# Optimization experiments

Hardware: AMD Instinct MI355X
Metric: run time of the kernel (lower is better)

The kernel has to match this reference:

```python
import jax, jax.numpy as jnp
import numpy as np

H_DIM = 1024


def setup_inputs() -> dict:
    key = jax.random.key(0)
    k1, k2, k3, k4 = jax.random.split(key, 4)
    B, S, H = 8, 2048, H_DIM
    scale = 1.0 / np.sqrt(H)
    x = jax.random.normal(k1, (B, S, H), dtype=jnp.float32)
    attention_mask = jnp.ones((B, S), dtype=jnp.int32)
    wq = jax.random.normal(k2, (H, H), dtype=jnp.float32) * scale
    wk = jax.random.normal(k3, (H, H), dtype=jnp.float32) * scale
    wv = jax.random.normal(k4, (H, H), dtype=jnp.float32) * scale
    return {"x": x, "attention_mask": attention_mask, "wq": wq, "wk": wk, "wv": wv}


def reference(x, attention_mask, wq, wk, wv):
    # x: [B,S,H]; torch Linear(no bias): y = x @ W.T
    B, S, H = x.shape
    q = jnp.einsum('bsh,oh->bso', x, wq)
    k = jnp.einsum('bsh,oh->bso', x, wk)
    v = jnp.einsum('bsh,oh->bso', x, wv)
    qk = jnp.einsum('bqh,bkh->bqk', q, k) / jnp.sqrt(jnp.asarray(H, jnp.float32))
    # causal: mask positions where key index > query index (strict upper triangle)
    causal = jnp.triu(jnp.ones((S, S), dtype=bool), k=1)  # [S,S]
    m = attention_mask.astype(bool)                        # [B,S]
    allowed = m[:, None, :] & m[:, :, None]                # d & e: key-valid AND query-valid
    condition = causal[None, :, :] | jnp.logical_not(allowed)
    qk = jnp.where(condition, -jnp.inf, qk)
    att = jax.nn.softmax(qk, axis=-1)
    att = jnp.where(jnp.isnan(att), 0.0, att)  # fully-masked rows -> 0
    return jnp.einsum('bqk,bkh->bqh', att, v)
```

## Files before the change

### kernel.cpp

```cpp
#include <hip/hip_runtime.h>
#include <stdint.h>

typedef unsigned short u16;
typedef __bf16 bf16x8 __attribute__((ext_vector_type(8)));
typedef float f32x4 __attribute__((ext_vector_type(4)));
typedef u16 ushort8 __attribute__((ext_vector_type(8)));

#define SB 8
#define SS 2048
#define SH 1024
#define MTOT (SB*SS)
#define LOG2E 1.44269504088896f
#define SEXP (1.44269504088896f/32.f)
#define NEG_INF (-__builtin_inff())

typedef __attribute__((address_space(3))) void lds_void;
typedef __attribute__((address_space(1))) const void gbl_void;

__device__ __forceinline__ float bf2f(u16 v) {
    union { unsigned int u; float f; } x; x.u = ((unsigned int)v) << 16; return x.f;
}
__device__ __forceinline__ u16 f2bf(float f) {
    unsigned int u = __builtin_bit_cast(unsigned int, f);
    u += 0x7fffu + ((u >> 16) & 1u);
    return (u16)(u >> 16);
}

__global__ void cvt_f32_bf16(const float* __restrict__ in, u16* __restrict__ out, int n8) {
    int i = blockIdx.x * 256 + threadIdx.x;
    if (i >= n8) return;
    const float4* p = (const float4*)(in + (size_t)i * 8);
    float4 a = p[0], b = p[1];
    ushort8 r;
    r[0] = f2bf(a.x); r[1] = f2bf(a.y); r[2] = f2bf(a.z); r[3] = f2bf(a.w);
    r[4] = f2bf(b.x); r[5] = f2bf(b.y); r[6] = f2bf(b.z); r[7] = f2bf(b.w);
    *(ushort8*)(out + (size_t)i * 8) = r;
}

__device__ __forceinline__ void stage_tile(const u16* __restrict__ g, int ld,
                                           u16* lds, int w, int l) {
#pragma unroll
    for (int i = 0; i < 4; i++) {
        int chunk = i * 4 + w;
        int r = chunk * 8 + (l >> 3);
        int c = (l & 7) * 8;
        __builtin_amdgcn_global_load_lds(
            (gbl_void*)(g + (size_t)r * ld + c),
            (lds_void*)(lds + chunk * 512), 16, 0, 0);
    }
}

__device__ __forceinline__ void mfma_tile(const u16* As, const u16* Bs,
                                          f32x4 acc[4][4], int w, int l) {
    int wr = (w >> 1) * 64, wc = (w & 1) * 64;
    int lr = l & 15, lk = (l >> 4) * 8;
#pragma unroll
    for (int kk = 0; kk < 2; kk++) {
        bf16x8 af[4], bb[4];
#pragma unroll
        for (int m = 0; m < 4; m++)
            af[m] = *(const bf16x8*)(const void*)(As + (wr + m * 16 + lr) * 64 + kk * 32 + lk);
#pragma unroll
        for (int n = 0; n < 4; n++)
            bb[n] = *(const bf16x8*)(const void*)(Bs + (wc + n * 16 + lr) * 64 + kk * 32 + lk);
#pragma unroll
        for (int m = 0; m < 4; m++)
#pragma unroll
            for (int n = 0; n < 4; n++)
                acc[m][n] = __builtin_amdgcn_mfma_f32_16x16x32_bf16(af[m], bb[n], acc[m][n], 0, 0, 0);
    }
}

#define QNT 16

#define STAGE8(gbase, ld, bufidx, h, t) do {                                          \
    const u16* _g = (gbase) + ((size_t)((h)*128 + srow)) * (ld) + (size_t)(t)*64 + scol; \
    u16* _d = &lds4[bufidx][((h)*128 + (w << 3)) * 64];                               \
    __builtin_amdgcn_global_load_lds((gbl_void*)_g, (lds_void*)_d, 16, 0, 0);         \
    __builtin_amdgcn_global_load_lds((gbl_void*)(_g + (size_t)64*(ld)),               \
                                     (lds_void*)(_d + 64*64), 16, 0, 0);              \
} while (0)

#define LDA8(mf, kkv) (*(const bf16x8*)(const void*)(Ab + (wr + (mf)*16 + rrow)*64 + rk##kkv))
#define LDB8(nf, kkv) (*(const bf16x8*)(const void*)(Bb + (wc + (nf)*16 + rrow)*64 + rk##kkv))

#define MFMA_PAIR(mf, A0, A1)                                                          \
    acc[mf][0] = __builtin_amdgcn_mfma_f32_16x16x32_bf16(A0, b00, acc[mf][0], 0,0,0);  \
    acc[mf][0] = __builtin_amdgcn_mfma_f32_16x16x32_bf16(A1, b01, acc[mf][0], 0,0,0);  \
    acc[mf][1] = __builtin_amdgcn_mfma_f32_16x16x32_bf16(A0, b10, acc[mf][1], 0,0,0);  \
    acc[mf][1] = __builtin_amdgcn_mfma_f32_16x16x32_bf16(A1, b11, acc[mf][1], 0,0,0);  \
    acc[mf][2] = __builtin_amdgcn_mfma_f32_16x16x32_bf16(A0, b20, acc[mf][2], 0,0,0);  \
    acc[mf][2] = __builtin_amdgcn_mfma_f32_16x16x32_bf16(A1, b21, acc[mf][2], 0,0,0);  \
    acc[mf][3] = __builtin_amdgcn_mfma_f32_16x16x32_bf16(A0, b30, acc[mf][3], 0,0,0);  \
    acc[mf][3] = __builtin_amdgcn_mfma_f32_16x16x32_bf16(A1, b31, acc[mf][3], 0,0,0);

#define PH_BAR_MID()                       \
    __builtin_amdgcn_sched_barrier(0);     \
    __builtin_amdgcn_s_barrier();          \
    __builtin_amdgcn_sched_barrier(0);

#define PH_BAR_END()                       \
    __builtin_amdgcn_sched_barrier(0);     \
    __builtin_amdgcn_s_barrier();          \
    __builtin_amdgcn_sched_barrier(0);

__global__ __launch_bounds__(512, 2) void gemm_qkv8(
    const u16* __restrict__ X, const u16* __restrict__ W,
    u16* __restrict__ Q, u16* __restrict__ Kd, u16* __restrict__ Vd) {
    __shared__ u16 lds4[4][256 * 64];

    int tid = threadIdx.x, w = tid >> 6, l = tid & 63;
    int bid = blockIdx.x;
    int wg = (bid & 7) * 96 + (bid >> 3);
    int mt = wg / 12, nb = wg % 12;

    const u16* gA = X + (size_t)mt * 256 * SH;
    const u16* gB = W + (size_t)nb * 256 * SH;

    int srow = (w << 3) + (l >> 3);
    int scol = (((l & 7) ^ ((l >> 3) & 7)) << 3);
    int wr = (w >> 2) * 128, wc = (w & 3) * 64;
    int rrow = l & 15;
    int rk0 = (((l >> 4) ^ (l & 7)) << 3);
    int rk1 = (((4 + (l >> 4)) ^ (l & 7)) << 3);

    f32x4 acc[8][4];
#pragma unroll
    for (int m = 0; m < 8; m++)
#pragma unroll
        for (int n = 0; n < 4; n++) acc[m][n] = (f32x4){0.f, 0.f, 0.f, 0.f};

    STAGE8(gA, SH, 0, 0, 0); STAGE8(gA, SH, 0, 1, 0);
    STAGE8(gB, SH, 2, 0, 0); STAGE8(gB, SH, 2, 1, 0);
    STAGE8(gB, SH, 3, 0, 1); STAGE8(gB, SH, 3, 1, 1);
    asm volatile("s_waitcnt vmcnt(4)" ::: "memory");
    __builtin_amdgcn_s_barrier();
    __builtin_amdgcn_sched_barrier(0);

    for (int t = 0; t < QNT; ++t) {
        const int p = t & 1;
        const u16* Ab = &lds4[p][0];
        const u16* Bb = &lds4[2 + p][0];

        bf16x8 b00 = LDB8(0, 0), b01 = LDB8(0, 1), b10 = LDB8(1, 0), b11 = LDB8(1, 1);
        bf16x8 b20 = LDB8(2, 0), b21 = LDB8(2, 1), b30 = LDB8(3, 0), b31 = LDB8(3, 1);
        {
            bf16x8 a00 = LDA8(0, 0), a01 = LDA8(0, 1), a10 = LDA8(1, 0), a11 = LDA8(1, 1);
            if (t + 1 < QNT) STAGE8(gA, SH, (t + 1) & 1, 0, t + 1);
            PH_BAR_MID();
            __builtin_amdgcn_s_setprio(1);
            MFMA_PAIR(0, a00, a01);
            MFMA_PAIR(1, a10, a11);
            __builtin_amdgcn_s_setprio(0);
            PH_BAR_END();
        }
        {
            bf16x8 a00 = LDA8(2, 0), a01 = LDA8(2, 1), a10 = LDA8(3, 0), a11 = LDA8(3, 1);
            if (t + 1 < QNT) STAGE8(gA, SH, (t + 1) & 1, 1, t + 1);
            PH_BAR_MID();
            __builtin_amdgcn_s_setprio(1);
            MFMA_PAIR(2, a00, a01);
            MFMA_PAIR(3, a10, a11);
            __builtin_amdgcn_s_setprio(0);
            PH_BAR_END();
        }
        {
            bf16x8 a00 = LDA8(4, 0), a01 = LDA8(4, 1), a10 = LDA8(5, 0), a11 = LDA8(5, 1);
            if (t + 2 < QNT) STAGE8(gB, SH, 2 + (t & 1), 0, t + 2);
            PH_BAR_MID();
            __builtin_amdgcn_s_setprio(1);
            MFMA_PAIR(4, a00, a01);
            MFMA_PAIR(5, a10, a11);
            __builtin_amdgcn_s_setprio(0);
            PH_BAR_END();
        }
        {
            bf16x8 a00 = LDA8(6, 0), a01 = LDA8(6, 1), a10 = LDA8(7, 0), a11 = LDA8(7, 1);
            if (t + 2 < QNT) STAGE8(gB, SH, 2 + (t & 1), 1, t + 2);
            if (t + 2 < QNT)      asm volatile("s_waitcnt vmcnt(4)" ::: "memory");
            else if (t + 1 < QNT) asm volatile("s_waitcnt vmcnt(0)" ::: "memory");
            PH_BAR_MID();
            __builtin_amdgcn_s_setprio(1);
            MFMA_PAIR(6, a00, a01);
            MFMA_PAIR(7, a10, a11);
            __builtin_amdgcn_s_setprio(0);
            PH_BAR_END();
        }
    }

    u16* outp = (nb < 4 ? Q : (nb < 8 ? Kd : Vd));
    int colbase = (nb & 3) * 256 + wc;
    size_t rowbase = (size_t)mt * 256 + wr;
    int g = l >> 4, c = l & 15;
#pragma unroll
    for (int mf = 0; mf < 8; mf++)
#pragma unroll
        for (int j = 0; j < 4; j++) {
            size_t ro = (rowbase + mf * 16 + g * 4 + j) * SH;
#pragma unroll
            for (int nf = 0; nf < 4; nf++)
                outp[ro + colbase + nf * 16 + c] = f2bf(acc[mf][nf][j]);
        }
}

__global__ void transpose_v(const u16* __restrict__ V, u16* __restrict__ Vt) {
    __shared__ u16 t[64][80];
    int s0 = blockIdx.x * 64, o0 = blockIdx.y * 64, b = blockIdx.z;
    const u16* src = V + (size_t)b * SS * SH;
    u16* dst = Vt + (size_t)b * SH * SS;
    int tid = threadIdx.x;
#pragma unroll
    for (int it = 0; it < 2; it++) {
        int idx = it * 256 + tid;
        int r = idx >> 3, gq = idx & 7;
        *(ushort8*)&t[r][gq * 8] = *(const ushort8*)&src[(size_t)(s0 + r) * SH + o0 + gq * 8];
    }
    __syncthreads();
#pragma unroll
    for (int it = 0; it < 2; it++) {
        int idx = it * 256 + tid;
        int rr = idx >> 3, cc = idx & 7;
        ushort8 v;
#pragma unroll
        for (int e = 0; e < 8; e++) v[e] = t[cc * 8 + e][rr];
        *(ushort8*)&dst[(size_t)(o0 + rr) * SS + s0 + cc * 8] = v;
    }
}

__global__ __launch_bounds__(256, 2) void gemm_scores(
    const u16* __restrict__ Q, const u16* __restrict__ K,
    u16* __restrict__ P, float* __restrict__ lb,
    const int* __restrict__ amask) {
    __shared__ u16 As[128 * 64];
    __shared__ u16 Bs[128 * 64];
    int tid = threadIdx.x, w = tid >> 6, l = tid & 63;
    int b = blockIdx.y, t = blockIdx.x;
    int qt = (int)((sqrtf(8.f * (float)t + 1.f) - 1.f) * 0.5f);
    while ((qt + 1) * (qt + 2) / 2 <= t) qt++;
    while (qt * (qt + 1) / 2 > t) qt--;
    int kt = t - qt * (qt + 1) / 2;
    const u16* A = Q + ((size_t)b * SS + (size_t)qt * 128) * SH;
    const u16* Bt = K + ((size_t)b * SS + (size_t)kt * 128) * SH;
    f32x4 acc[4][4];
#pragma unroll
    for (int m = 0; m < 4; m++)
#pragma unroll
        for (int n = 0; n < 4; n++) acc[m][n] = (f32x4){0.f, 0.f, 0.f, 0.f};
    for (int k0 = 0; k0 < SH; k0 += 64) {
        stage_tile(A + k0, SH, As, w, l);
        stage_tile(Bt + k0, SH, Bs, w, l);
        __syncthreads();
        mfma_tile(As, Bs, acc, w, l);
        __syncthreads();
    }
    int wr = (w >> 1) * 64, wc = (w & 1) * 64, g = l >> 4, c = l & 15;
    int q0 = qt * 128 + wr;
    int k0w = kt * 128 + wc;
    int cglob = kt * 2 + (w & 1);
    u16* Pb = P + (size_t)b * SS * SS;
    float* lbb = lb + (size_t)b * SS * 32;
    int kg[4], kv[4];
#pragma unroll
    for (int n = 0; n < 4; n++) { kg[n] = k0w + n * 16 + c; kv[n] = amask[b * SS + kg[n]]; }
#pragma unroll
    for (int m = 0; m < 4; m++) {
#pragma unroll
        for (int j = 0; j < 4; j++) {
            int qg = q0 + m * 16 + g * 4 + j;
            float sv[4]; float ls = 0.f;
#pragma unroll
            for (int n = 0; n < 4; n++) {
                bool ok = (kg[n] <= qg) && (kv[n] != 0);
                float p = ok ? exp2f(acc[m][n][j] * SEXP) : 0.f;
                sv[n] = p; ls += p;
            }
#pragma unroll
            for (int d = 1; d < 16; d <<= 1) ls += __shfl_xor(ls, d, 64);
            size_t prow = (size_t)qg * SS;
#pragma unroll
            for (int n = 0; n < 4; n++) Pb[prow + kg[n]] = f2bf(sv[n]);
            if (c == 0) lbb[(size_t)qg * 32 + cglob] = ls;
        }
    }
}

__global__ void combine_inv(const float* __restrict__ lb,
                            float* __restrict__ sb, const int* __restrict__ amask) {
    int row = blockIdx.x * 4 + (threadIdx.x >> 6);
    int l = threadIdx.x & 63;
    int b = row >> 11, q = row & 2047;
    int cmax = q >> 6;
    float L = (l < 32 && l <= cmax) ? lb[(size_t)row * 32 + l] : 0.f;
#pragma unroll
    for (int d = 1; d < 64; d <<= 1) L += __shfl_xor(L, d, 64);
    if (l == 0) {
        int qv = amask[b * SS + q];
        sb[row] = (qv != 0 && L > 0.f) ? 1.0f / L : 0.f;
    }
}

__global__ __launch_bounds__(256, 2) void gemm_pv(
    const u16* __restrict__ P, const u16* __restrict__ Vt,
    const float* __restrict__ sb, float* __restrict__ Out) {
    __shared__ u16 As[128 * 64];
    __shared__ u16 Bs[128 * 64];
    int tid = threadIdx.x, w = tid >> 6, l = tid & 63;
    int b = blockIdx.y;
    int qt = blockIdx.x >> 3, nt = blockIdx.x & 7;
    const u16* Ab = P + (size_t)b * SS * SS + (size_t)qt * 128 * SS;
    const u16* Bt = Vt + (size_t)b * SH * SS + (size_t)nt * 128 * SS;
    int ksize = (qt + 1) * 128;
    f32x4 acc[4][4];
#pragma unroll
    for (int m = 0; m < 4; m++)
#pragma unroll
        for (int n = 0; n < 4; n++) acc[m][n] = (f32x4){0.f, 0.f, 0.f, 0.f};
    for (int k0 = 0; k0 < ksize; k0 += 64) {
        stage_tile(Ab + k0, SS, As, w, l);
        stage_tile(Bt + k0, SS, Bs, w, l);
        __syncthreads();
        mfma_tile(As, Bs, acc, w, l);
        __syncthreads();
    }
    const float* sbq = sb + (size_t)b * SS + (size_t)qt * 128;
    float* out = Out + ((size_t)b * SS + (size_t)qt * 128) * SH + nt * 128;
    int wr = (w >> 1) * 64, wc = (w & 1) * 64, g = l >> 4, c = l & 15;
#pragma unroll
    for (int m = 0; m < 4; m++)
#pragma unroll
        for (int j = 0; j < 4; j++) {
            int row = wr + m * 16 + g * 4 + j;
            float scl = sbq[row];
            size_t ro = (size_t)row * SH;
#pragma unroll
            for (int n = 0; n < 4; n++)
                out[ro + wc + n * 16 + c] = acc[m][n][j] * scl;
        }
}

extern "C" void kernel_launch(void* const* d_in, const int* in_sizes, int n_in,
                              void* d_out, int out_size, void* d_ws, size_t ws_size,
                              hipStream_t stream) {
    const float* x = (const float*)d_in[0];
    const int* amask = (const int*)d_in[1];
    const float* wq = (const float*)d_in[2];
    const float* wk = (const float*)d_in[3];
    const float* wv = (const float*)d_in[4];
    float* out = (float*)d_out;

    const size_t SZQ = (size_t)MTOT * SH * 2;
    const size_t SZSTAT = (size_t)MTOT * 32 * 4;
    char* ws = (char*)d_ws;
    u16* Q   = (u16*)(ws);
    u16* Kb  = (u16*)(ws + SZQ);
    u16* V   = (u16*)(ws + 2 * SZQ);
    u16* Vt  = (u16*)(ws + 3 * SZQ);
    float* lb = (float*)(ws + 4 * SZQ);
    float* sb = (float*)(ws + 4 * SZQ + SZSTAT);
    u16* P   = (u16*)(ws + 4 * SZQ + 3 * SZSTAT);
    u16* xb  = P;
    u16* wb  = P + (size_t)MTOT * SH;

    cvt_f32_bf16<<<8192, 256, 0, stream>>>(x, xb, MTOT * SH / 8);
    cvt_f32_bf16<<<512, 256, 0, stream>>>(wq, wb, SH * SH / 8);
    cvt_f32_bf16<<<512, 256, 0, stream>>>(wk, wb + (size_t)SH * SH, SH * SH / 8);
    cvt_f32_bf16<<<512, 256, 0, stream>>>(wv, wb + (size_t)2 * SH * SH, SH * SH / 8);

    gemm_qkv8<<<768, 512, 0, stream>>>(xb, wb, Q, Kb, V);
    transpose_v<<<dim3(32, 16, 8), 256, 0, stream>>>(V, Vt);
    gemm_scores<<<dim3(136, 8), 256, 0, stream>>>(Q, Kb, P, lb, amask);
    combine_inv<<<4096, 256, 0, stream>>>(lb, sb, amask);
    gemm_pv<<<dim3(128, 8), 256, 0, stream>>>(P, Vt, sb, out);
}
```

Before: 395.2 us.

## Fuse conversions, merge QKV phases, stage epilogue via LDS, remap grids

Merges the four f32-to-bf16 conversion launches into one kernel. In the QKV GEMM main loop it collapses four barrier-separated phases into two, issuing both stage loads together. The QKV output epilogue now goes through LDS so each thread writes 16-byte coalesced stores instead of scattered 2-byte stores. The scores and PV kernels get a 1D grid that interleaves batches across XCD-adjacent block IDs, and PV schedules the longest causal query tiles first. Costs are higher register pressure from holding more A fragments per phase, plus extra LDS passes and barriers in the epilogue.

New measurement: 348.3 us. 11.9% less time.

```diff
diff --git a/kernel.cpp b/kernel.cpp
--- a/kernel.cpp
+++ b/kernel.cpp
@@ -12,7 +12,6 @@
 #define MTOT (SB*SS)
 #define LOG2E 1.44269504088896f
 #define SEXP (1.44269504088896f/32.f)
-#define NEG_INF (-__builtin_inff())
 
 typedef __attribute__((address_space(3))) void lds_void;
 typedef __attribute__((address_space(1))) const void gbl_void;
@@ -26,15 +25,22 @@
     return (u16)(u >> 16);
 }
 
-__global__ void cvt_f32_bf16(const float* __restrict__ in, u16* __restrict__ out, int n8) {
+__global__ void cvt_all(const float* __restrict__ x,  const float* __restrict__ wq,
+                        const float* __restrict__ wk, const float* __restrict__ wv,
+                        u16* __restrict__ xb, u16* __restrict__ wb) {
+    const int NX = MTOT * SH / 8, NW = SH * SH / 8;
     int i = blockIdx.x * 256 + threadIdx.x;
-    if (i >= n8) return;
-    const float4* p = (const float4*)(in + (size_t)i * 8);
+    const float* src; u16* dst; int off;
+    if (i < NX)               { src = x;  dst = xb;                        off = i; }
+    else if (i < NX + NW)     { src = wq; dst = wb;                        off = i - NX; }
+    else if (i < NX + 2 * NW) { src = wk; dst = wb + (size_t)SH * SH;      off = i - NX - NW; }
+    else                      { src = wv; dst = wb + (size_t)2 * SH * SH;  off = i - NX - 2 * NW; }
+    const float4* p = (const float4*)(src + (size_t)off * 8);
     float4 a = p[0], b = p[1];
     ushort8 r;
     r[0] = f2bf(a.x); r[1] = f2bf(a.y); r[2] = f2bf(a.z); r[3] = f2bf(a.w);
     r[4] = f2bf(b.x); r[5] = f2bf(b.y); r[6] = f2bf(b.z); r[7] = f2bf(b.w);
-    *(ushort8*)(out + (size_t)i * 8) = r;
+    *(ushort8*)(dst + (size_t)off * 8) = r;
 }
 
 __device__ __forceinline__ void stage_tile(const u16* __restrict__ g, int ld,
@@ -146,61 +152,63 @@
         bf16x8 b20 = LDB8(2, 0), b21 = LDB8(2, 1), b30 = LDB8(3, 0), b31 = LDB8(3, 1);
         {
             bf16x8 a00 = LDA8(0, 0), a01 = LDA8(0, 1), a10 = LDA8(1, 0), a11 = LDA8(1, 1);
-            if (t + 1 < QNT) STAGE8(gA, SH, (t + 1) & 1, 0, t + 1);
+            bf16x8 a20 = LDA8(2, 0), a21 = LDA8(2, 1), a30 = LDA8(3, 0), a31 = LDA8(3, 1);
+            if (t + 1 < QNT) { STAGE8(gA, SH, (t + 1) & 1, 0, t + 1); STAGE8(gA, SH, (t + 1) & 1, 1, t + 1); }
             PH_BAR_MID();
             __builtin_amdgcn_s_setprio(1);
             MFMA_PAIR(0, a00, a01);
             MFMA_PAIR(1, a10, a11);
+            MFMA_PAIR(2, a20, a21);
+            MFMA_PAIR(3, a30, a31);
             __builtin_amdgcn_s_setprio(0);
             PH_BAR_END();
         }
         {
-            bf16x8 a00 = LDA8(2, 0), a01 = LDA8(2, 1), a10 = LDA8(3, 0), a11 = LDA8(3, 1);
-            if (t + 1 < QNT) STAGE8(gA, SH, (t + 1) & 1, 1, t + 1);
-            PH_BAR_MID();
-            __builtin_amdgcn_s_setprio(1);
-            MFMA_PAIR(2, a00, a01);
-            MFMA_PAIR(3, a10, a11);
-            __builtin_amdgcn_s_setprio(0);
-            PH_BAR_END();
-        }
-        {
             bf16x8 a00 = LDA8(4, 0), a01 = LDA8(4, 1), a10 = LDA8(5, 0), a11 = LDA8(5, 1);
-            if (t + 2 < QNT) STAGE8(gB, SH, 2 + (t & 1), 0, t + 2);
+            bf16x8 a20 = LDA8(6, 0), a21 = LDA8(6, 1), a30 = LDA8(7, 0), a31 = LDA8(7, 1);
+            if (t + 2 < QNT) { STAGE8(gB, SH, 2 + (t & 1), 0, t + 2); STAGE8(gB, SH, 2 + (t & 1), 1, t + 2); }
+            if (t + 2 < QNT)      asm volatile("s_waitcnt vmcnt(4)" ::: "memory");
+            else if (t + 1 < QNT) asm volatile("s_waitcnt vmcnt(0)" ::: "memory");
             PH_BAR_MID();
             __builtin_amdgcn_s_setprio(1);
             MFMA_PAIR(4, a00, a01);
             MFMA_PAIR(5, a10, a11);
+            MFMA_PAIR(6, a20, a21);
+            MFMA_PAIR(7, a30, a31);
             __builtin_amdgcn_s_setprio(0);
             PH_BAR_END();
         }
-        {
-            bf16x8 a00 = LDA8(6, 0), a01 = LDA8(6, 1), a10 = LDA8(7, 0), a11 = LDA8(7, 1);
-            if (t + 2 < QNT) STAGE8(gB, SH, 2 + (t & 1), 1, t + 2);
-            if (t + 2 < QNT)      asm volatile("s_waitcnt vmcnt(4)" ::: "memory");
-            else if (t + 1 < QNT) asm volatile("s_waitcnt vmcnt(0)" ::: "memory");
-            PH_BAR_MID();
-            __builtin_amdgcn_s_setprio(1);
-            MFMA_PAIR(6, a00, a01);
-            MFMA_PAIR(7, a10, a11);
-            __builtin_amdgcn_s_setprio(0);
-            PH_BAR_END();
-        }
     }
 
     u16* outp = (nb < 4 ? Q : (nb < 8 ? Kd : Vd));
-    int colbase = (nb & 3) * 256 + wc;
-    size_t rowbase = (size_t)mt * 256 + wr;
+    size_t colb = (size_t)(nb & 3) * 256;
     int g = l >> 4, c = l & 15;
-#pragma unroll
-    for (int mf = 0; mf < 8; mf++)
-#pragma unroll
-        for (int j = 0; j < 4; j++) {
-            size_t ro = (rowbase + mf * 16 + g * 4 + j) * SH;
-#pragma unroll
-            for (int nf = 0; nf < 4; nf++)
-                outp[ro + colbase + nf * 16 + c] = f2bf(acc[mf][nf][j]);
-        }
+    u16* S = &lds4[0][0];
+    __syncthreads();
+#pragma unroll
+    for (int pass = 0; pass < 2; ++pass) {
+        if ((w >> 2) == pass) {
+#pragma unroll
+            for (int mf = 0; mf < 8; mf++)
+#pragma unroll
+                for (int j = 0; j < 4; j++) {
+                    int rl = mf * 16 + g * 4 + j;
+#pragma unroll
+                    for (int nf = 0; nf < 4; nf++)
+                        S[rl * 264 + wc + nf * 16 + c] = f2bf(acc[mf][nf][j]);
+                }
+        }
+        __syncthreads();
+#pragma unroll
+        for (int q8 = 0; q8 < 8; ++q8) {
+            int idx = q8 * 4096 + tid * 8;
+            int row = idx >> 8;
+            int colu = idx & 255;
+            *(ushort8*)(outp + ((size_t)(mt * 256 + pass * 128 + row)) * SH + colb + colu)
+                = *(const ushort8*)(S + row * 264 + colu);
+        }
+        __syncthreads();
+    }
 }
 
 __global__ void transpose_v(const u16* __restrict__ V, u16* __restrict__ Vt) {
@@ -234,7 +242,9 @@
     __shared__ u16 As[128 * 64];
     __shared__ u16 Bs[128 * 64];
     int tid = threadIdx.x, w = tid >> 6, l = tid & 63;
-    int b = blockIdx.y, t = blockIdx.x;
+    int x = blockIdx.x;
+    int wk_ = (x & 7) * 136 + (x >> 3);
+    int b = wk_ / 136, t = wk_ % 136;
     int qt = (int)((sqrtf(8.f * (float)t + 1.f) - 1.f) * 0.5f);
     while ((qt + 1) * (qt + 2) / 2 <= t) qt++;
     while (qt * (qt + 1) / 2 > t) qt--;
@@ -305,8 +315,11 @@
     __shared__ u16 As[128 * 64];
     __shared__ u16 Bs[128 * 64];
     int tid = threadIdx.x, w = tid >> 6, l = tid & 63;
-    int b = blockIdx.y;
-    int qt = blockIdx.x >> 3, nt = blockIdx.x & 7;
+    int x = blockIdx.x;
+    int wk_ = (x & 7) * 128 + (x >> 3);
+    int b = wk_ >> 7;
+    int r7 = wk_ & 127;
+    int qt = 15 - (r7 >> 3), nt = r7 & 7;
     const u16* Ab = P + (size_t)b * SS * SS + (size_t)qt * 128 * SS;
     const u16* Bt = Vt + (size_t)b * SH * SS + (size_t)nt * 128 * SS;
     int ksize = (qt + 1) * 128;
@@ -361,14 +374,11 @@
     u16* xb  = P;
     u16* wb  = P + (size_t)MTOT * SH;
 
-    cvt_f32_bf16<<<8192, 256, 0, stream>>>(x, xb, MTOT * SH / 8);
-    cvt_f32_bf16<<<512, 256, 0, stream>>>(wq, wb, SH * SH / 8);
-    cvt_f32_bf16<<<512, 256, 0, stream>>>(wk, wb + (size_t)SH * SH, SH * SH / 8);
-    cvt_f32_bf16<<<512, 256, 0, stream>>>(wv, wb + (size_t)2 * SH * SH, SH * SH / 8);
+    cvt_all<<<9728, 256, 0, stream>>>(x, wq, wk, wv, xb, wb);
 
     gemm_qkv8<<<768, 512, 0, stream>>>(xb, wb, Q, Kb, V);
     transpose_v<<<dim3(32, 16, 8), 256, 0, stream>>>(V, Vt);
-    gemm_scores<<<dim3(136, 8), 256, 0, stream>>>(Q, Kb, P, lb, amask);
+    gemm_scores<<<1088, 256, 0, stream>>>(Q, Kb, P, lb, amask);
     combine_inv<<<4096, 256, 0, stream>>>(lb, sb, amask);
-    gemm_pv<<<dim3(128, 8), 256, 0, stream>>>(P, Vt, sb, out);
-}
+    gemm_pv<<<1024, 256, 0, stream>>>(P, Vt, sb, out);
+}
```
